# Kernel tuning notes

Hardware: AMD Instinct MI355X
Metric: run time of the kernel (lower is better)

Reference implementation:

```python
import jax, jax.numpy as jnp
import numpy as np

N_NODES = 8192
N_EDGES = 262144
FEAT = 128


def _lin(key, fan_in, fan_out):
    k1, k2 = jax.random.split(key)
    s = 1.0 / np.sqrt(fan_in)
    w = jax.random.uniform(k1, (fan_in, fan_out), jnp.float32, -s, s)
    b = jax.random.uniform(k2, (fan_out,), jnp.float32, -s, s)
    return w, b


def setup_inputs() -> dict:
    key = jax.random.key(0)
    ks = jax.random.split(key, 16)
    adj = jax.random.randint(ks[0], (2, N_EDGES), 0, N_NODES)
    features = jax.random.normal(ks[1], (N_NODES, FEAT), jnp.float32)
    w1, b1 = _lin(ks[2], FEAT, 64)
    w2, b2 = _lin(ks[3], 64, 32)
    w3, b3 = _lin(ks[4], 32, 32)
    # MultiheadAttention params (embed_dim=32, 1 head)
    kq = jax.random.split(ks[5], 2)
    wqkv = jax.random.uniform(kq[0], (96, 32), jnp.float32, -1/np.sqrt(32), 1/np.sqrt(32))
    bqkv = jnp.zeros((96,), jnp.float32)
    wo = jax.random.uniform(kq[1], (32, 32), jnp.float32, -1/np.sqrt(32), 1/np.sqrt(32))
    bo = jnp.zeros((32,), jnp.float32)
    w4, b4 = _lin(ks[6], 32, 32)
    w5a, b5a = _lin(ks[7], 32, 32)
    w6a, b6a = _lin(ks[8], 32, 64)
    w7a, b7a = _lin(ks[9], 64, 2)
    w5f, b5f = _lin(ks[10], 32, 32)
    w6f, b6f = _lin(ks[11], 32, 64)
    w7f, b7f = _lin(ks[12], 64, FEAT)
    return dict(adj=adj, features=features, w1=w1, b1=b1, w2=w2, b2=b2, w3=w3, b3=b3,
                wqkv=wqkv, bqkv=bqkv, wo=wo, bo=bo, w4=w4, b4=b4,
                w5a=w5a, b5a=b5a, w6a=w6a, b6a=b6a, w7a=w7a, b7a=b7a,
                w5f=w5f, b5f=b5f, w6f=w6f, b6f=b6f, w7f=w7f, b7f=b7f)


def _gcn(x, w, b, src, dst, norm, n):
    # PyG GCNConv: out = scatter_add(norm * (x W)[src] -> dst) + b
    h = x @ w
    return jax.ops.segment_sum(h[src] * norm[:, None], dst, num_segments=n) + b


def reference(adj, features, w1, b1, w2, b2, w3, b3, wqkv, bqkv, wo, bo, w4, b4,
              w5a, b5a, w6a, b6a, w7a, b7a, w5f, b5f, w6f, b6f, w7f, b7f):
    n = features.shape[0]
    loops = jnp.arange(n)
    src = jnp.concatenate([adj[0], loops])  # self-loops added (gcn_norm)
    dst = jnp.concatenate([adj[1], loops])
    deg = jax.ops.segment_sum(jnp.ones_like(src, jnp.float32), dst, num_segments=n)
    dinv = jnp.where(deg > 0, jax.lax.rsqrt(deg), 0.0)
    norm = dinv[src] * dinv[dst]

    h = jax.nn.relu(_gcn(features, w1, b1, src, dst, norm, n))
    h = jax.nn.relu(_gcn(h, w2, b2, src, dst, norm, n))
    h = jax.nn.relu(_gcn(h, w3, b3, src, dst, norm, n))

    # single-head self-attention over all nodes (seq_len=n, batch=1)
    qkv = h @ wqkv.T + bqkv
    q, k, v = jnp.split(qkv, 3, axis=-1)  # [n,32] each
    attn = jax.nn.softmax((q @ k.T) * (1.0 / np.sqrt(32.0)), axis=-1)  # [n,n]
    h = (attn @ v) @ wo.T + bo

    h = jax.nn.relu(_gcn(h, w4, b4, src, dst, norm, n))

    da = jax.nn.relu(_gcn(h, w5a, b5a, src, dst, norm, n))
    da = jax.nn.relu(_gcn(da, w6a, b6a, src, dst, norm, n))
    da = jax.nn.relu(_gcn(da, w7a, b7a, src, dst, norm, n))  # [n,2]

    df = jax.nn.relu(_gcn(h, w5f, b5f, src, dst, norm, n))
    df = jax.nn.relu(_gcn(df, w6f, b6f, src, dst, norm, n))
    df = jax.nn.relu(_gcn(df, w7f, b7f, src, dst, norm, n))  # [n,FEAT]
    return (da, df)
```

## Files before the change

### kernel.cpp

```cpp
#include <hip/hip_runtime.h>

#define N_NODES 8192
#define N_EDGES 262144

typedef __attribute__((ext_vector_type(4))) float f32x4;
typedef _Float16 half8 __attribute__((ext_vector_type(8)));
typedef __fp16 fp16x2 __attribute__((ext_vector_type(2)));
union UH { half8 h8; fp16x2 h2[4]; };
union HC { _Float16 h; unsigned short u; };


__global__ void __launch_bounds__(256) count_kernel(const int* __restrict__ dst,
                                                    int* __restrict__ cnt) {
  int e = blockIdx.x * 256 + threadIdx.x;
  atomicAdd(&cnt[dst[e]], 1);
}

__global__ void __launch_bounds__(1024) scan_kernel(const int* __restrict__ cnt,
                                                    int* __restrict__ rp,
                                                    float* __restrict__ dinv) {
  __shared__ int sums[1024];
  const int t = threadIdx.x;
  const int base = t * 8;
  int c[8];
  int s = 0;
#pragma unroll
  for (int i = 0; i < 8; ++i) { c[i] = cnt[base + i]; s += c[i]; }
  sums[t] = s;
  __syncthreads();
  for (int off = 1; off < 1024; off <<= 1) {
    int v = (t >= off) ? sums[t - off] : 0;
    __syncthreads();
    sums[t] += v;
    __syncthreads();
  }
  int run = (t == 0) ? 0 : sums[t - 1];
#pragma unroll
  for (int i = 0; i < 8; ++i) {
    rp[base + i] = run;
    run += c[i];
    dinv[base + i] = rsqrtf((float)(c[i] + 1));
  }
  if (t == 1023) rp[N_NODES] = run;
}

__global__ void __launch_bounds__(256) fill_kernel(const int* __restrict__ src,
                                                   const int* __restrict__ dst,
                                                   const int* __restrict__ rp,
                                                   const float* __restrict__ dinv,
                                                   int* __restrict__ cur,
                                                   int* __restrict__ col,
                                                   float* __restrict__ wgt) {
  int e = blockIdx.x * 256 + threadIdx.x;
  int d = dst[e], s = src[e];
  int p = atomicAdd(&cur[d], 1);
  int at = rp[d] + p;
  col[at] = s;
  wgt[at] = dinv[s] * dinv[d];
}


template <int FIN, int FOUT, bool WT, bool BIAS, bool RELU>
__device__ __forceinline__ void mm_body(const float* __restrict__ x,
                                        const float* __restrict__ w,
                                        const float* __restrict__ bias,
                                        float* __restrict__ out, int bx, int tid,
                                        float* ws, float* xs) {
  constexpr int VEC = (FOUT >= 32) ? 4 : 1;
  constexpr int TC = FOUT / VEC;
  constexpr int ROWS = 256 / TC;
  const int r0 = bx * ROWS;
  for (int i = tid; i < FIN * FOUT; i += 256) {
    int k = i / FOUT, j = i % FOUT;
    ws[i] = WT ? w[j * FIN + k] : w[i];
  }
  for (int i = tid; i < ROWS * FIN; i += 256) {
    int r = i / FIN, k = i % FIN;
    xs[r * (FIN + 1) + k] = x[(size_t)(r0 + r) * FIN + k];
  }
  __syncthreads();
  const int jc = tid % TC, r = tid / TC;
  float acc[VEC];
#pragma unroll
  for (int v = 0; v < VEC; ++v) acc[v] = 0.0f;
#pragma unroll
  for (int k = 0; k < FIN; ++k) {
    const float xv = xs[r * (FIN + 1) + k];
#pragma unroll
    for (int v = 0; v < VEC; ++v) acc[v] += xv * ws[k * FOUT + jc * VEC + v];
  }
#pragma unroll
  for (int v = 0; v < VEC; ++v) {
    int j = jc * VEC + v;
    float o = BIAS ? (acc[v] + bias[j]) : acc[v];
    if (RELU) o = fmaxf(o, 0.0f);
    out[(size_t)(r0 + r) * FOUT + j] = o;
  }
}

template <int FIN, int FOUT, bool WT, bool BIAS, bool RELU = false>
__global__ void __launch_bounds__(256) mm_kernel(const float* __restrict__ x,
                                                 const float* __restrict__ w,
                                                 const float* __restrict__ bias,
                                                 float* __restrict__ out) {
  constexpr int VEC = (FOUT >= 32) ? 4 : 1;
  constexpr int ROWS = 256 / (FOUT / VEC);
  __shared__ float ws[FIN * FOUT];
  __shared__ float xs[ROWS * (FIN + 1)];
  mm_body<FIN, FOUT, WT, BIAS, RELU>(x, w, bias, out, blockIdx.x, threadIdx.x, ws, xs);
}

template <int FIN, int FOUT, bool WT, bool BIAS, bool RELU, int G>
__global__ void __launch_bounds__(256) mm_dual_kernel(
    const float* __restrict__ xA, const float* __restrict__ wA,
    const float* __restrict__ bA, float* __restrict__ outA,
    const float* __restrict__ xB, const float* __restrict__ wB,
    const float* __restrict__ bB, float* __restrict__ outB) {
  constexpr int VEC = (FOUT >= 32) ? 4 : 1;
  constexpr int ROWS = 256 / (FOUT / VEC);
  __shared__ float ws[FIN * FOUT];
  __shared__ float xs[ROWS * (FIN + 1)];
  if (blockIdx.x < G)
    mm_body<FIN, FOUT, WT, BIAS, RELU>(xA, wA, bA, outA, blockIdx.x, threadIdx.x, ws, xs);
  else
    mm_body<FIN, FOUT, WT, BIAS, RELU>(xB, wB, bB, outB, blockIdx.x - G, threadIdx.x, ws, xs);
}


template <int F, bool BR>
__device__ __forceinline__ void aggv_body(const float* __restrict__ t,
                                          const int* __restrict__ rp,
                                          const int* __restrict__ col,
                                          const float* __restrict__ wgt,
                                          const float* __restrict__ dinv,
                                          const float* __restrict__ bias,
                                          float* __restrict__ out, int bx, int tid) {
  constexpr int TPN = F / 4;
  constexpr int EPI = 64 / TPN;
  const int wv = tid >> 6;
  const int lane = tid & 63;
  const int n = bx * 4 + wv;
  const int eo = lane / TPN;
  const int fq = lane % TPN;
  const float di = dinv[n];
  const int rs = rp[n], re = rp[n + 1];
  f32x4 acc = {0.f, 0.f, 0.f, 0.f};
  if (eo == 0) {
    const f32x4 tv = *(const f32x4*)&t[(size_t)n * F + fq * 4];
    acc = di * di * tv;
  }
  for (int e = rs + eo; e < re; e += EPI) {
    const int c = col[e];
    const float w = wgt[e];
    const f32x4 tv = *(const f32x4*)&t[(size_t)c * F + fq * 4];
    acc += w * tv;
  }
#pragma unroll
  for (int off = TPN; off < 64; off <<= 1) {
    acc[0] += __shfl_xor(acc[0], off, 64);
    acc[1] += __shfl_xor(acc[1], off, 64);
    acc[2] += __shfl_xor(acc[2], off, 64);
    acc[3] += __shfl_xor(acc[3], off, 64);
  }
  if (eo == 0) {
    f32x4 r = acc;
    if (BR) {
      const f32x4 bv = *(const f32x4*)&bias[fq * 4];
      r = acc + bv;
      r[0] = fmaxf(r[0], 0.f); r[1] = fmaxf(r[1], 0.f);
      r[2] = fmaxf(r[2], 0.f); r[3] = fmaxf(r[3], 0.f);
    }
    *(f32x4*)&out[(size_t)n * F + fq * 4] = r;
  }
}

template <int F, bool BR = true>
__global__ void __launch_bounds__(256) aggv_kernel(const float* __restrict__ t,
                                                   const int* __restrict__ rp,
                                                   const int* __restrict__ col,
                                                   const float* __restrict__ wgt,
                                                   const float* __restrict__ dinv,
                                                   const float* __restrict__ bias,
                                                   float* __restrict__ out) {
  aggv_body<F, BR>(t, rp, col, wgt, dinv, bias, out, blockIdx.x, threadIdx.x);
}

template <int F, bool BR, int G>
__global__ void __launch_bounds__(256) aggv_dual_kernel(
    const float* __restrict__ tA, const float* __restrict__ bA, float* __restrict__ outA,
    const float* __restrict__ tB, const float* __restrict__ bB, float* __restrict__ outB,
    const int* __restrict__ rp, const int* __restrict__ col,
    const float* __restrict__ wgt, const float* __restrict__ dinv) {
  if (blockIdx.x < G)
    aggv_body<F, BR>(tA, rp, col, wgt, dinv, bA, outA, blockIdx.x, threadIdx.x);
  else
    aggv_body<F, BR>(tB, rp, col, wgt, dinv, bB, outB, blockIdx.x - G, threadIdx.x);
}

template <int F>
__global__ void __launch_bounds__(256) agg_kernel(const float* __restrict__ t,
                                                  const int* __restrict__ rp,
                                                  const int* __restrict__ col,
                                                  const float* __restrict__ wgt,
                                                  const float* __restrict__ dinv,
                                                  const float* __restrict__ bias,
                                                  float* __restrict__ out) {
  constexpr int NPB = 256 / F;
  const int tid = threadIdx.x;
  const int n = blockIdx.x * NPB + tid / F;
  const int f = tid % F;
  const float di = dinv[n];
  float acc = di * di * t[(size_t)n * F + f];
  const int rs = rp[n], re = rp[n + 1];
  for (int e = rs; e < re; ++e) {
    acc += wgt[e] * t[(size_t)col[e] * F + f];
  }
  acc += bias[f];
  out[(size_t)n * F + f] = fmaxf(acc, 0.0f);
}


__global__ void __launch_bounds__(256) qkv_kernel(const float* __restrict__ x,
                                                  const float* __restrict__ wqkv,
                                                  const float* __restrict__ bqkv,
                                                  unsigned short* __restrict__ Q16,
                                                  unsigned short* __restrict__ K16,
                                                  unsigned short* __restrict__ V16) {
  __shared__ float wls[96 * 33];
  __shared__ float xs[8 * 33];
  const int tid = threadIdx.x;
  const int r = tid >> 5, j = tid & 31;
  const int row = blockIdx.x * 8 + r;
  for (int i = tid; i < 96 * 32; i += 256) wls[(i >> 5) * 33 + (i & 31)] = wqkv[i];
  xs[(tid >> 5) * 33 + (tid & 31)] = x[(size_t)(blockIdx.x * 8 + (tid >> 5)) * 32 + (tid & 31)];
  __syncthreads();
  float aq = bqkv[j], ak = bqkv[32 + j], av = bqkv[64 + j];
#pragma unroll
  for (int k = 0; k < 32; ++k) {
    const float xv = xs[r * 33 + k];
    aq += xv * wls[j * 33 + k];
    ak += xv * wls[(32 + j) * 33 + k];
    av += xv * wls[(64 + j) * 33 + k];
  }
  const float QSCALE = 1.4426950408889634f * 0.17677669529663687f;
  aq *= QSCALE;
  HC cq, ck, cv;
  cq.h = (_Float16)aq;
  ck.h = (_Float16)ak;
  cv.h = (_Float16)av;
  Q16[row * 32 + j] = cq.u;
  K16[row * 32 + j] = ck.u;
  const int ko = row & 31;
  const int slot = 8 * ((ko & 15) >> 2) + ((ko >> 4) << 2) + (ko & 3);
  V16[j * N_NODES + (row & ~31) + slot] = cv.u;
}


__device__ __forceinline__ void wave_writeout(float (*lds)[544], float (*wexp)[16],
                                              float* Mq, float* Lq, const f32x4& o1,
                                              const f32x4& o2, float m, float l, int wid,
                                              int g, int li, int tid, int qt, int by,
                                              float* __restrict__ part) {
#pragma unroll
  for (int r = 0; r < 4; ++r) {
    lds[wid][(4 * g + r) * 16 + li] = o1[r];
    lds[wid][(16 + 4 * g + r) * 16 + li] = o2[r];
  }
  if (g == 0) {
    lds[wid][512 + li] = m;
    lds[wid][528 + li] = l;
  }
  __syncthreads();
  if (tid < 16) {
    const int q = tid;
    const float m0 = lds[0][512 + q], m1 = lds[1][512 + q];
    const float m2 = lds[2][512 + q], m3 = lds[3][512 + q];
    const float M = fmaxf(fmaxf(m0, m1), fmaxf(m2, m3));
    const float w0 = exp2f(m0 - M), w1 = exp2f(m1 - M);
    const float w2 = exp2f(m2 - M), w3 = exp2f(m3 - M);
    wexp[0][q] = w0; wexp[1][q] = w1; wexp[2][q] = w2; wexp[3][q] = w3;
    Mq[q] = M;
    Lq[q] = w0 * lds[0][528 + q] + w1 * lds[1][528 + q] +
            w2 * lds[2][528 + q] + w3 * lds[3][528 + q];
  }
  __syncthreads();
  const int base = (qt * 4 + by) * 544;
#pragma unroll
  for (int e2 = 0; e2 < 2; ++e2) {
    const int e = tid + e2 * 256;
    const int q = e & 15;
    part[base + e] = wexp[0][q] * lds[0][e] + wexp[1][q] * lds[1][e] +
                     wexp[2][q] * lds[2][e] + wexp[3][q] * lds[3][e];
  }
  if (tid < 16) {
    part[base + 512 + tid] = Mq[tid];
    part[base + 528 + tid] = Lq[tid];
  }
}

__global__ void __launch_bounds__(256, 4) attn_mfma_kernel(
    const unsigned short* __restrict__ Q16, const unsigned short* __restrict__ K16,
    const unsigned short* __restrict__ V16, float* __restrict__ part) {
  __shared__ float lds[4][544];
  __shared__ float wexp[4][16];
  __shared__ float Mq[16], Lq[16];
  const int tid = threadIdx.x;
  const int wid = tid >> 6;
  const int lane = tid & 63;
  const int g = lane >> 4;
  const int li = lane & 15;
  const int qpair = blockIdx.x;
  const int q0A = qpair * 32;
  const int q0B = q0A + 16;
  const int kbeg = blockIdx.y * 2048 + wid * 512;

  const half8 qfA = *(const half8*)&Q16[(q0A + li) * 32 + 8 * g];
  const half8 qfB = *(const half8*)&Q16[(q0B + li) * 32 + 8 * g];
  const int koff = li * 32 + 8 * g;
  const int vA = li * N_NODES + 8 * g;
  const int vB = (16 + li) * N_NODES + 8 * g;

  f32x4 oAA = {0.f, 0.f, 0.f, 0.f}, oBA = {0.f, 0.f, 0.f, 0.f};
  f32x4 oAB = {0.f, 0.f, 0.f, 0.f}, oBB = {0.f, 0.f, 0.f, 0.f};
  float mA = -1e30f, lA = 0.f, mB = -1e30f, lB = 0.f;

  for (int t = kbeg; t < kbeg + 512; t += 64) {
    const half8 k0 = *(const half8*)&K16[(t)*32 + koff];
    const half8 k1 = *(const half8*)&K16[(t + 16) * 32 + koff];
    const half8 k2 = *(const half8*)&K16[(t + 32) * 32 + koff];
    const half8 k3 = *(const half8*)&K16[(t + 48) * 32 + koff];
    const half8 va0 = *(const half8*)&V16[vA + t];
    const half8 vb0 = *(const half8*)&V16[vB + t];
    const half8 va1 = *(const half8*)&V16[vA + t + 32];
    const half8 vb1 = *(const half8*)&V16[vB + t + 32];

    {
      f32x4 s0 = {0.f, 0.f, 0.f, 0.f}, s1 = {0.f, 0.f, 0.f, 0.f};
      f32x4 s2 = {0.f, 0.f, 0.f, 0.f}, s3 = {0.f, 0.f, 0.f, 0.f};
      s0 = __builtin_amdgcn_mfma_f32_16x16x32_f16(k0, qfA, s0, 0, 0, 0);
      s1 = __builtin_amdgcn_mfma_f32_16x16x32_f16(k1, qfA, s1, 0, 0, 0);
      s2 = __builtin_amdgcn_mfma_f32_16x16x32_f16(k2, qfA, s2, 0, 0, 0);
      s3 = __builtin_amdgcn_mfma_f32_16x16x32_f16(k3, qfA, s3, 0, 0, 0);
      float mxl = fmaxf(fmaxf(fmaxf(s0[0], s0[1]), fmaxf(s0[2], s0[3])),
                        fmaxf(fmaxf(s1[0], s1[1]), fmaxf(s1[2], s1[3])));
      mxl = fmaxf(mxl, fmaxf(fmaxf(fmaxf(s2[0], s2[1]), fmaxf(s2[2], s2[3])),
                             fmaxf(fmaxf(s3[0], s3[1]), fmaxf(s3[2], s3[3]))));
      if (!__all(mxl <= mA)) {
        float mx = mxl;
        mx = fmaxf(mx, __shfl_xor(mx, 16, 64));
        mx = fmaxf(mx, __shfl_xor(mx, 32, 64));
        const float mn = fmaxf(mA, mx);
        const float fct = exp2f(mA - mn);
        oAA *= fct; oBA *= fct; lA *= fct;
        mA = mn;
      }
      const float p0 = exp2f(s0[0] - mA), p1 = exp2f(s0[1] - mA);
      const float p2 = exp2f(s0[2] - mA), p3 = exp2f(s0[3] - mA);
      const float p4 = exp2f(s1[0] - mA), p5 = exp2f(s1[1] - mA);
      const float p6 = exp2f(s1[2] - mA), p7 = exp2f(s1[3] - mA);
      const float p8 = exp2f(s2[0] - mA), p9 = exp2f(s2[1] - mA);
      const float pa = exp2f(s2[2] - mA), pb = exp2f(s2[3] - mA);
      const float pc = exp2f(s3[0] - mA), pd = exp2f(s3[1] - mA);
      const float pe = exp2f(s3[2] - mA), pf = exp2f(s3[3] - mA);
      lA += (((p0 + p1) + (p2 + p3)) + ((p4 + p5) + (p6 + p7))) +
            (((p8 + p9) + (pa + pb)) + ((pc + pd) + (pe + pf)));
      UH ph0, ph1;
      ph0.h2[0] = __builtin_amdgcn_cvt_pkrtz(p0, p1);
      ph0.h2[1] = __builtin_amdgcn_cvt_pkrtz(p2, p3);
      ph0.h2[2] = __builtin_amdgcn_cvt_pkrtz(p4, p5);
      ph0.h2[3] = __builtin_amdgcn_cvt_pkrtz(p6, p7);
      ph1.h2[0] = __builtin_amdgcn_cvt_pkrtz(p8, p9);
      ph1.h2[1] = __builtin_amdgcn_cvt_pkrtz(pa, pb);
      ph1.h2[2] = __builtin_amdgcn_cvt_pkrtz(pc, pd);
      ph1.h2[3] = __builtin_amdgcn_cvt_pkrtz(pe, pf);
      oAA = __builtin_amdgcn_mfma_f32_16x16x32_f16(va0, ph0.h8, oAA, 0, 0, 0);
      oAA = __builtin_amdgcn_mfma_f32_16x16x32_f16(va1, ph1.h8, oAA, 0, 0, 0);
      oBA = __builtin_amdgcn_mfma_f32_16x16x32_f16(vb0, ph0.h8, oBA, 0, 0, 0);
      oBA = __builtin_amdgcn_mfma_f32_16x16x32_f16(vb1, ph1.h8, oBA, 0, 0, 0);
    }
    {
      f32x4 s0 = {0.f, 0.f, 0.f, 0.f}, s1 = {0.f, 0.f, 0.f, 0.f};
      f32x4 s2 = {0.f, 0.f, 0.f, 0.f}, s3 = {0.f, 0.f, 0.f, 0.f};
      s0 = __builtin_amdgcn_mfma_f32_16x16x32_f16(k0, qfB, s0, 0, 0, 0);
      s1 = __builtin_amdgcn_mfma_f32_16x16x32_f16(k1, qfB, s1, 0, 0, 0);
      s2 = __builtin_amdgcn_mfma_f32_16x16x32_f16(k2, qfB, s2, 0, 0, 0);
      s3 = __builtin_amdgcn_mfma_f32_16x16x32_f16(k3, qfB, s3, 0, 0, 0);
      float mxl = fmaxf(fmaxf(fmaxf(s0[0], s0[1]), fmaxf(s0[2], s0[3])),
                        fmaxf(fmaxf(s1[0], s1[1]), fmaxf(s1[2], s1[3])));
      mxl = fmaxf(mxl, fmaxf(fmaxf(fmaxf(s2[0], s2[1]), fmaxf(s2[2], s2[3])),
                             fmaxf(fmaxf(s3[0], s3[1]), fmaxf(s3[2], s3[3]))));
      if (!__all(mxl <= mB)) {
        float mx = mxl;
        mx = fmaxf(mx, __shfl_xor(mx, 16, 64));
        mx = fmaxf(mx, __shfl_xor(mx, 32, 64));
        const float mn = fmaxf(mB, mx);
        const float fct = exp2f(mB - mn);
        oAB *= fct; oBB *= fct; lB *= fct;
        mB = mn;
      }
      const float p0 = exp2f(s0[0] - mB), p1 = exp2f(s0[1] - mB);
      const float p2 = exp2f(s0[2] - mB), p3 = exp2f(s0[3] - mB);
      const float p4 = exp2f(s1[0] - mB), p5 = exp2f(s1[1] - mB);
      const float p6 = exp2f(s1[2] - mB), p7 = exp2f(s1[3] - mB);
      const float p8 = exp2f(s2[0] - mB), p9 = exp2f(s2[1] - mB);
      const float pa = exp2f(s2[2] - mB), pb = exp2f(s2[3] - mB);
      const float pc = exp2f(s3[0] - mB), pd = exp2f(s3[1] - mB);
      const float pe = exp2f(s3[2] - mB), pf = exp2f(s3[3] - mB);
      lB += (((p0 + p1) + (p2 + p3)) + ((p4 + p5) + (p6 + p7))) +
            (((p8 + p9) + (pa + pb)) + ((pc + pd) + (pe + pf)));
      UH ph0, ph1;
      ph0.h2[0] = __builtin_amdgcn_cvt_pkrtz(p0, p1);
      ph0.h2[1] = __builtin_amdgcn_cvt_pkrtz(p2, p3);
      ph0.h2[2] = __builtin_amdgcn_cvt_pkrtz(p4, p5);
      ph0.h2[3] = __builtin_amdgcn_cvt_pkrtz(p6, p7);
      ph1.h2[0] = __builtin_amdgcn_cvt_pkrtz(p8, p9);
      ph1.h2[1] = __builtin_amdgcn_cvt_pkrtz(pa, pb);
      ph1.h2[2] = __builtin_amdgcn_cvt_pkrtz(pc, pd);
      ph1.h2[3] = __builtin_amdgcn_cvt_pkrtz(pe, pf);
      oAB = __builtin_amdgcn_mfma_f32_16x16x32_f16(va0, ph0.h8, oAB, 0, 0, 0);
      oAB = __builtin_amdgcn_mfma_f32_16x16x32_f16(va1, ph1.h8, oAB, 0, 0, 0);
      oBB = __builtin_amdgcn_mfma_f32_16x16x32_f16(vb0, ph0.h8, oBB, 0, 0, 0);
      oBB = __builtin_amdgcn_mfma_f32_16x16x32_f16(vb1, ph1.h8, oBB, 0, 0, 0);
    }
  }

  lA += __shfl_xor(lA, 16, 64);
  lA += __shfl_xor(lA, 32, 64);
  lB += __shfl_xor(lB, 16, 64);
  lB += __shfl_xor(lB, 32, 64);

  wave_writeout(lds, wexp, Mq, Lq, oAA, oBA, mA, lA, wid, g, li, tid, qpair * 2,
                blockIdx.y, part);
  __syncthreads();
  wave_writeout(lds, wexp, Mq, Lq, oAB, oBB, mB, lB, wid, g, li, tid, qpair * 2 + 1,
                blockIdx.y, part);
}


__global__ void __launch_bounds__(256) attn_combine_wo(const float* __restrict__ part,
                                                       const float* __restrict__ wo,
                                                       const float* __restrict__ bo,
                                                       float* __restrict__ out) {
  __shared__ float wols[1024];
  __shared__ float bos[32];
  __shared__ float aos[4][16][33];
  const int tid = threadIdx.x;
  for (int i = tid; i < 1024; i += 256) wols[i] = wo[i];
  if (tid < 32) bos[tid] = bo[tid];
  const int wv = tid >> 6, lane = tid & 63;
  const int qt = blockIdx.x * 4 + wv;
  const int q = lane & 15, g = lane >> 4;
  const int pb = qt * 4 * 544;
  const float m0 = part[pb + 512 + q], m1 = part[pb + 544 + 512 + q];
  const float m2 = part[pb + 1088 + 512 + q], m3 = part[pb + 1632 + 512 + q];
  const float M = fmaxf(fmaxf(m0, m1), fmaxf(m2, m3));
  const float w0 = exp2f(m0 - M), w1 = exp2f(m1 - M);
  const float w2 = exp2f(m2 - M), w3 = exp2f(m3 - M);
  const float L = w0 * part[pb + 528 + q] + w1 * part[pb + 544 + 528 + q] +
                  w2 * part[pb + 1088 + 528 + q] + w3 * part[pb + 1632 + 528 + q];
  const float invL = 1.0f / L;
#pragma unroll
  for (int r = 0; r < 8; ++r) {
    const int d = g + 4 * r;
    const int o = d * 16 + q;
    const float ov = w0 * part[pb + o] + w1 * part[pb + 544 + o] +
                     w2 * part[pb + 1088 + o] + w3 * part[pb + 1632 + o];
    aos[wv][q][d] = ov * invL;
  }
  __syncthreads();
#pragma unroll
  for (int r = 0; r < 8; ++r) {
    const int dout = g + 4 * r;
    float acc = bos[dout];
#pragma unroll
    for (int k = 0; k < 32; ++k) acc += aos[wv][q][k] * wols[dout * 32 + k];
    out[(size_t)(qt * 16 + q) * 32 + dout] = acc;
  }
}


extern "C" void kernel_launch(void* const* d_in, const int* in_sizes, int n_in,
                              void* d_out, int out_size, void* d_ws, size_t ws_size,
                              hipStream_t stream) {
  (void)in_sizes; (void)n_in; (void)out_size; (void)ws_size;
  const int* adj = (const int*)d_in[0];
  const float* feat = (const float*)d_in[1];
  const float* w1 = (const float*)d_in[2];  const float* b1 = (const float*)d_in[3];
  const float* w2 = (const float*)d_in[4];  const float* b2 = (const float*)d_in[5];
  const float* w3 = (const float*)d_in[6];  const float* b3 = (const float*)d_in[7];
  const float* wqkv = (const float*)d_in[8];const float* bqkv = (const float*)d_in[9];
  const float* wo = (const float*)d_in[10]; const float* bo = (const float*)d_in[11];
  const float* w4 = (const float*)d_in[12]; const float* b4 = (const float*)d_in[13];
  const float* w5a = (const float*)d_in[14];const float* b5a = (const float*)d_in[15];
  const float* w6a = (const float*)d_in[16];const float* b6a = (const float*)d_in[17];
  const float* w7a = (const float*)d_in[18];const float* b7a = (const float*)d_in[19];
  const float* w5f = (const float*)d_in[20];const float* b5f = (const float*)d_in[21];
  const float* w6f = (const float*)d_in[22];const float* b6f = (const float*)d_in[23];
  const float* w7f = (const float*)d_in[24];const float* b7f = (const float*)d_in[25];
  float* outp = (float*)d_out;

  float* wsf = (float*)d_ws;
  int* wsi = (int*)d_ws;
  int* cnt = wsi;
  int* cur = wsi + 8192;
  int* rp = wsi + 16384;
  float* dinv = wsf + 24832;
  float* wgt = wsf + 33024;
  int* col = wsi + 295168;
  float* T = wsf + 557312;
  float* T2 = T + 262144;
  float* B0 = wsf + 1605888;
  float* B1 = wsf + 2130176;
  float* B2 = wsf + 2392320;
  unsigned short* Q16 = (unsigned short*)(wsf + 2916608);
  unsigned short* K16 = Q16 + 262144;
  unsigned short* V16 = K16 + 262144;
  float* part = T;

  const int* src = adj;
  const int* dst = adj + N_EDGES;

  hipMemsetAsync(cnt, 0, 2 * N_NODES * sizeof(int), stream);
  count_kernel<<<N_EDGES / 256, 256, 0, stream>>>(dst, cnt);
  scan_kernel<<<1, 1024, 0, stream>>>(cnt, rp, dinv);
  fill_kernel<<<N_EDGES / 256, 256, 0, stream>>>(src, dst, rp, dinv, cur, col, wgt);

  mm_kernel<128, 64, false, false><<<N_NODES / 16, 256, 0, stream>>>(feat, w1, nullptr, T);
  aggv_kernel<64><<<N_NODES / 4, 256, 0, stream>>>(T, rp, col, wgt, dinv, b1, B0);
  mm_kernel<64, 32, false, false><<<N_NODES / 32, 256, 0, stream>>>(B0, w2, nullptr, T);
  aggv_kernel<32><<<N_NODES / 4, 256, 0, stream>>>(T, rp, col, wgt, dinv, b2, B1);
  mm_kernel<32, 32, false, false><<<N_NODES / 32, 256, 0, stream>>>(B1, w3, nullptr, T);
  aggv_kernel<32><<<N_NODES / 4, 256, 0, stream>>>(T, rp, col, wgt, dinv, b3, B0);

  qkv_kernel<<<N_NODES / 8, 256, 0, stream>>>(B0, wqkv, bqkv, Q16, K16, V16);
  {
    dim3 grid(256, 4);
    attn_mfma_kernel<<<grid, 256, 0, stream>>>(Q16, K16, V16, part);
  }
  attn_combine_wo<<<128, 256, 0, stream>>>(part, wo, bo, B2);

  mm_kernel<32, 32, false, false><<<N_NODES / 32, 256, 0, stream>>>(B2, w4, nullptr, T);
  aggv_kernel<32><<<N_NODES / 4, 256, 0, stream>>>(T, rp, col, wgt, dinv, b4, B0);

  mm_dual_kernel<32, 32, false, false, false, 256><<<512, 256, 0, stream>>>(
      B0, w5a, nullptr, T, B0, w5f, nullptr, T2);
  aggv_dual_kernel<32, true, 2048><<<4096, 256, 0, stream>>>(
      T, b5a, B1, T2, b5f, B2, rp, col, wgt, dinv);
  aggv_dual_kernel<32, false, 2048><<<4096, 256, 0, stream>>>(
      B1, nullptr, T, B2, nullptr, T2, rp, col, wgt, dinv);
  mm_dual_kernel<32, 64, false, true, true, 512><<<1024, 256, 0, stream>>>(
      T, w6a, b6a, B0, T2, w6f, b6f, B2);
  mm_kernel<64, 2, false, false><<<N_NODES / 128, 256, 0, stream>>>(B0, w7a, nullptr, B1);
  agg_kernel<2><<<N_NODES / 128, 256, 0, stream>>>(B1, rp, col, wgt, dinv, b7a, outp);
  aggv_kernel<64, false><<<N_NODES / 4, 256, 0, stream>>>(B2, rp, col, wgt, dinv, nullptr, T);
  mm_kernel<64, 128, false, true, true><<<N_NODES / 8, 256, 0, stream>>>(T, w7f, b7f,
                                                                         outp + 16384);
}
```

Baseline: 199.1 us.

## Process four query tiles per attention wave to reuse K/V loads; replace memset

```diff
diff --git a/kernel.cpp b/kernel.cpp
--- a/kernel.cpp
+++ b/kernel.cpp
@@ -8,6 +8,11 @@
 typedef __fp16 fp16x2 __attribute__((ext_vector_type(2)));
 union UH { half8 h8; fp16x2 h2[4]; };
 union HC { _Float16 h; unsigned short u; };
+
+
+__global__ void __launch_bounds__(256) zero_kernel(int4* __restrict__ p) {
+  p[blockIdx.x * 256 + threadIdx.x] = make_int4(0, 0, 0, 0);
+}
 
 
 __global__ void __launch_bounds__(256) count_kernel(const int* __restrict__ dst,
@@ -298,7 +303,53 @@
   }
 }
 
-__global__ void __launch_bounds__(256, 4) attn_mfma_kernel(
+#define ATTN_QTILE(QQ)                                                                \
+  do {                                                                                \
+    f32x4 s0 = {0.f, 0.f, 0.f, 0.f}, s1 = {0.f, 0.f, 0.f, 0.f};                      \
+    f32x4 s2 = {0.f, 0.f, 0.f, 0.f}, s3 = {0.f, 0.f, 0.f, 0.f};                      \
+    s0 = __builtin_amdgcn_mfma_f32_16x16x32_f16(k0, qf[QQ], s0, 0, 0, 0);             \
+    s1 = __builtin_amdgcn_mfma_f32_16x16x32_f16(k1, qf[QQ], s1, 0, 0, 0);             \
+    s2 = __builtin_amdgcn_mfma_f32_16x16x32_f16(k2, qf[QQ], s2, 0, 0, 0);             \
+    s3 = __builtin_amdgcn_mfma_f32_16x16x32_f16(k3, qf[QQ], s3, 0, 0, 0);             \
+    float mxl = fmaxf(fmaxf(fmaxf(s0[0], s0[1]), fmaxf(s0[2], s0[3])),                \
+                      fmaxf(fmaxf(s1[0], s1[1]), fmaxf(s1[2], s1[3])));               \
+    mxl = fmaxf(mxl, fmaxf(fmaxf(fmaxf(s2[0], s2[1]), fmaxf(s2[2], s2[3])),           \
+                           fmaxf(fmaxf(s3[0], s3[1]), fmaxf(s3[2], s3[3]))));         \
+    if (!__all(mxl <= m[QQ])) {                                                       \
+      float mx = mxl;                                                                 \
+      mx = fmaxf(mx, __shfl_xor(mx, 16, 64));                                         \
+      mx = fmaxf(mx, __shfl_xor(mx, 32, 64));                                         \
+      const float mn = fmaxf(m[QQ], mx);                                              \
+      const float fct = exp2f(m[QQ] - mn);                                            \
+      o1[QQ] *= fct; o2[QQ] *= fct; l[QQ] *= fct;                                     \
+      m[QQ] = mn;                                                                     \
+    }                                                                                 \
+    const float p0 = exp2f(s0[0] - m[QQ]), p1 = exp2f(s0[1] - m[QQ]);                 \
+    const float p2 = exp2f(s0[2] - m[QQ]), p3 = exp2f(s0[3] - m[QQ]);                 \
+    const float p4 = exp2f(s1[0] - m[QQ]), p5 = exp2f(s1[1] - m[QQ]);                 \
+    const float p6 = exp2f(s1[2] - m[QQ]), p7 = exp2f(s1[3] - m[QQ]);                 \
+    const float p8 = exp2f(s2[0] - m[QQ]), p9 = exp2f(s2[1] - m[QQ]);                 \
+    const float pa = exp2f(s2[2] - m[QQ]), pb = exp2f(s2[3] - m[QQ]);                 \
+    const float pc = exp2f(s3[0] - m[QQ]), pd = exp2f(s3[1] - m[QQ]);                 \
+    const float pe = exp2f(s3[2] - m[QQ]), pf = exp2f(s3[3] - m[QQ]);                 \
+    l[QQ] += (((p0 + p1) + (p2 + p3)) + ((p4 + p5) + (p6 + p7))) +                    \
+             (((p8 + p9) + (pa + pb)) + ((pc + pd) + (pe + pf)));                     \
+    UH ph0, ph1;                                                                      \
+    ph0.h2[0] = __builtin_amdgcn_cvt_pkrtz(p0, p1);                                   \
+    ph0.h2[1] = __builtin_amdgcn_cvt_pkrtz(p2, p3);                                   \
+    ph0.h2[2] = __builtin_amdgcn_cvt_pkrtz(p4, p5);                                   \
+    ph0.h2[3] = __builtin_amdgcn_cvt_pkrtz(p6, p7);                                   \
+    ph1.h2[0] = __builtin_amdgcn_cvt_pkrtz(p8, p9);                                   \
+    ph1.h2[1] = __builtin_amdgcn_cvt_pkrtz(pa, pb);                                   \
+    ph1.h2[2] = __builtin_amdgcn_cvt_pkrtz(pc, pd);                                   \
+    ph1.h2[3] = __builtin_amdgcn_cvt_pkrtz(pe, pf);                                   \
+    o1[QQ] = __builtin_amdgcn_mfma_f32_16x16x32_f16(va0, ph0.h8, o1[QQ], 0, 0, 0);    \
+    o1[QQ] = __builtin_amdgcn_mfma_f32_16x16x32_f16(va1, ph1.h8, o1[QQ], 0, 0, 0);    \
+    o2[QQ] = __builtin_amdgcn_mfma_f32_16x16x32_f16(vb0, ph0.h8, o2[QQ], 0, 0, 0);    \
+    o2[QQ] = __builtin_amdgcn_mfma_f32_16x16x32_f16(vb1, ph1.h8, o2[QQ], 0, 0, 0);    \
+  } while (0)
+
+__global__ void __launch_bounds__(256, 2) attn_mfma_kernel(
     const unsigned short* __restrict__ Q16, const unsigned short* __restrict__ K16,
     const unsigned short* __restrict__ V16, float* __restrict__ part) {
   __shared__ float lds[4][544];
@@ -309,20 +360,27 @@
   const int lane = tid & 63;
   const int g = lane >> 4;
   const int li = lane & 15;
-  const int qpair = blockIdx.x;
-  const int q0A = qpair * 32;
-  const int q0B = q0A + 16;
+  const int qquad = blockIdx.x;
   const int kbeg = blockIdx.y * 2048 + wid * 512;
 
-  const half8 qfA = *(const half8*)&Q16[(q0A + li) * 32 + 8 * g];
-  const half8 qfB = *(const half8*)&Q16[(q0B + li) * 32 + 8 * g];
+  half8 qf[4];
+#pragma unroll
+  for (int qq = 0; qq < 4; ++qq)
+    qf[qq] = *(const half8*)&Q16[(qquad * 64 + qq * 16 + li) * 32 + 8 * g];
+
   const int koff = li * 32 + 8 * g;
   const int vA = li * N_NODES + 8 * g;
   const int vB = (16 + li) * N_NODES + 8 * g;
 
-  f32x4 oAA = {0.f, 0.f, 0.f, 0.f}, oBA = {0.f, 0.f, 0.f, 0.f};
-  f32x4 oAB = {0.f, 0.f, 0.f, 0.f}, oBB = {0.f, 0.f, 0.f, 0.f};
-  float mA = -1e30f, lA = 0.f, mB = -1e30f, lB = 0.f;
+  f32x4 o1[4], o2[4];
+  float m[4], l[4];
+#pragma unroll
+  for (int qq = 0; qq < 4; ++qq) {
+    o1[qq] = f32x4{0.f, 0.f, 0.f, 0.f};
+    o2[qq] = f32x4{0.f, 0.f, 0.f, 0.f};
+    m[qq] = -1e30f;
+    l[qq] = 0.f;
+  }
 
   for (int t = kbeg; t < kbeg + 512; t += 64) {
     const half8 k0 = *(const half8*)&K16[(t)*32 + koff];
@@ -333,107 +391,29 @@
     const half8 vb0 = *(const half8*)&V16[vB + t];
     const half8 va1 = *(const half8*)&V16[vA + t + 32];
     const half8 vb1 = *(const half8*)&V16[vB + t + 32];
-
-    {
-      f32x4 s0 = {0.f, 0.f, 0.f, 0.f}, s1 = {0.f, 0.f, 0.f, 0.f};
-      f32x4 s2 = {0.f, 0.f, 0.f, 0.f}, s3 = {0.f, 0.f, 0.f, 0.f};
-      s0 = __builtin_amdgcn_mfma_f32_16x16x32_f16(k0, qfA, s0, 0, 0, 0);
-      s1 = __builtin_amdgcn_mfma_f32_16x16x32_f16(k1, qfA, s1, 0, 0, 0);
-      s2 = __builtin_amdgcn_mfma_f32_16x16x32_f16(k2, qfA, s2, 0, 0, 0);
-      s3 = __builtin_amdgcn_mfma_f32_16x16x32_f16(k3, qfA, s3, 0, 0, 0);
-      float mxl = fmaxf(fmaxf(fmaxf(s0[0], s0[1]), fmaxf(s0[2], s0[3])),
-                        fmaxf(fmaxf(s1[0], s1[1]), fmaxf(s1[2], s1[3])));
-      mxl = fmaxf(mxl, fmaxf(fmaxf(fmaxf(s2[0], s2[1]), fmaxf(s2[2], s2[3])),
-                             fmaxf(fmaxf(s3[0], s3[1]), fmaxf(s3[2], s3[3]))));
-      if (!__all(mxl <= mA)) {
-        float mx = mxl;
-        mx = fmaxf(mx, __shfl_xor(mx, 16, 64));
-        mx = fmaxf(mx, __shfl_xor(mx, 32, 64));
-        const float mn = fmaxf(mA, mx);
-        const float fct = exp2f(mA - mn);
-        oAA *= fct; oBA *= fct; lA *= fct;
-        mA = mn;
-      }
-      const float p0 = exp2f(s0[0] - mA), p1 = exp2f(s0[1] - mA);
-      const float p2 = exp2f(s0[2] - mA), p3 = exp2f(s0[3] - mA);
-      const float p4 = exp2f(s1[0] - mA), p5 = exp2f(s1[1] - mA);
-      const float p6 = exp2f(s1[2] - mA), p7 = exp2f(s1[3] - mA);
-      const float p8 = exp2f(s2[0] - mA), p9 = exp2f(s2[1] - mA);
-      const float pa = exp2f(s2[2] - mA), pb = exp2f(s2[3] - mA);
-      const float pc = exp2f(s3[0] - mA), pd = exp2f(s3[1] - mA);
-      const float pe = exp2f(s3[2] - mA), pf = exp2f(s3[3] - mA);
-      lA += (((p0 + p1) + (p2 + p3)) + ((p4 + p5) + (p6 + p7))) +
-            (((p8 + p9) + (pa + pb)) + ((pc + pd) + (pe + pf)));
-      UH ph0, ph1;
-      ph0.h2[0] = __builtin_amdgcn_cvt_pkrtz(p0, p1);
-      ph0.h2[1] = __builtin_amdgcn_cvt_pkrtz(p2, p3);
-      ph0.h2[2] = __builtin_amdgcn_cvt_pkrtz(p4, p5);
-      ph0.h2[3] = __builtin_amdgcn_cvt_pkrtz(p6, p7);
-      ph1.h2[0] = __builtin_amdgcn_cvt_pkrtz(p8, p9);
-      ph1.h2[1] = __builtin_amdgcn_cvt_pkrtz(pa, pb);
-      ph1.h2[2] = __builtin_amdgcn_cvt_pkrtz(pc, pd);
-      ph1.h2[3] = __builtin_amdgcn_cvt_pkrtz(pe, pf);
-      oAA = __builtin_amdgcn_mfma_f32_16x16x32_f16(va0, ph0.h8, oAA, 0, 0, 0);
-      oAA = __builtin_amdgcn_mfma_f32_16x16x32_f16(va1, ph1.h8, oAA, 0, 0, 0);
-      oBA = __builtin_amdgcn_mfma_f32_16x16x32_f16(vb0, ph0.h8, oBA, 0, 0, 0);
-      oBA = __builtin_amdgcn_mfma_f32_16x16x32_f16(vb1, ph1.h8, oBA, 0, 0, 0);
-    }
-    {
-      f32x4 s0 = {0.f, 0.f, 0.f, 0.f}, s1 = {0.f, 0.f, 0.f, 0.f};
-      f32x4 s2 = {0.f, 0.f, 0.f, 0.f}, s3 = {0.f, 0.f, 0.f, 0.f};
-      s0 = __builtin_amdgcn_mfma_f32_16x16x32_f16(k0, qfB, s0, 0, 0, 0);
-      s1 = __builtin_amdgcn_mfma_f32_16x16x32_f16(k1, qfB, s1, 0, 0, 0);
-      s2 = __builtin_amdgcn_mfma_f32_16x16x32_f16(k2, qfB, s2, 0, 0, 0);
-      s3 = __builtin_amdgcn_mfma_f32_16x16x32_f16(k3, qfB, s3, 0, 0, 0);
-      float mxl = fmaxf(fmaxf(fmaxf(s0[0], s0[1]), fmaxf(s0[2], s0[3])),
-                        fmaxf(fmaxf(s1[0], s1[1]), fmaxf(s1[2], s1[3])));
-      mxl = fmaxf(mxl, fmaxf(fmaxf(fmaxf(s2[0], s2[1]), fmaxf(s2[2], s2[3])),
-                             fmaxf(fmaxf(s3[0], s3[1]), fmaxf(s3[2], s3[3]))));
-      if (!__all(mxl <= mB)) {
-        float mx = mxl;
-        mx = fmaxf(mx, __shfl_xor(mx, 16, 64));
-        mx = fmaxf(mx, __shfl_xor(mx, 32, 64));
-        const float mn = fmaxf(mB, mx);
-        const float fct = exp2f(mB - mn);
-        oAB *= fct; oBB *= fct; lB *= fct;
-        mB = mn;
-      }
-      const float p0 = exp2f(s0[0] - mB), p1 = exp2f(s0[1] - mB);
-      const float p2 = exp2f(s0[2] - mB), p3 = exp2f(s0[3] - mB);
-      const float p4 = exp2f(s1[0] - mB), p5 = exp2f(s1[1] - mB);
-      const float p6 = exp2f(s1[2] - mB), p7 = exp2f(s1[3] - mB);
-      const float p8 = exp2f(s2[0] - mB), p9 = exp2f(s2[1] - mB);
-      const float pa = exp2f(s2[2] - mB), pb = exp2f(s2[3] - mB);
-      const float pc = exp2f(s3[0] - mB), pd = exp2f(s3[1] - mB);
-      const float pe = exp2f(s3[2] - mB), pf = exp2f(s3[3] - mB);
-      lB += (((p0 + p1) + (p2 + p3)) + ((p4 + p5) + (p6 + p7))) +
-            (((p8 + p9) + (pa + pb)) + ((pc + pd) + (pe + pf)));
-      UH ph0, ph1;
-      ph0.h2[0] = __builtin_amdgcn_cvt_pkrtz(p0, p1);
-      ph0.h2[1] = __builtin_amdgcn_cvt_pkrtz(p2, p3);
-      ph0.h2[2] = __builtin_amdgcn_cvt_pkrtz(p4, p5);
-      ph0.h2[3] = __builtin_amdgcn_cvt_pkrtz(p6, p7);
-      ph1.h2[0] = __builtin_amdgcn_cvt_pkrtz(p8, p9);
-      ph1.h2[1] = __builtin_amdgcn_cvt_pkrtz(pa, pb);
-      ph1.h2[2] = __builtin_amdgcn_cvt_pkrtz(pc, pd);
-      ph1.h2[3] = __builtin_amdgcn_cvt_pkrtz(pe, pf);
-      oAB = __builtin_amdgcn_mfma_f32_16x16x32_f16(va0, ph0.h8, oAB, 0, 0, 0);
-      oAB = __builtin_amdgcn_mfma_f32_16x16x32_f16(va1, ph1.h8, oAB, 0, 0, 0);
-      oBB = __builtin_amdgcn_mfma_f32_16x16x32_f16(vb0, ph0.h8, oBB, 0, 0, 0);
-      oBB = __builtin_amdgcn_mfma_f32_16x16x32_f16(vb1, ph1.h8, oBB, 0, 0, 0);
-    }
-  }
-
-  lA += __shfl_xor(lA, 16, 64);
-  lA += __shfl_xor(lA, 32, 64);
-  lB += __shfl_xor(lB, 16, 64);
-  lB += __shfl_xor(lB, 32, 64);
-
-  wave_writeout(lds, wexp, Mq, Lq, oAA, oBA, mA, lA, wid, g, li, tid, qpair * 2,
-                blockIdx.y, part);
-  __syncthreads();
-  wave_writeout(lds, wexp, Mq, Lq, oAB, oBB, mB, lB, wid, g, li, tid, qpair * 2 + 1,
-                blockIdx.y, part);
+    ATTN_QTILE(0);
+    ATTN_QTILE(1);
+    ATTN_QTILE(2);
+    ATTN_QTILE(3);
+  }
+
+#pragma unroll
+  for (int qq = 0; qq < 4; ++qq) {
+    l[qq] += __shfl_xor(l[qq], 16, 64);
+    l[qq] += __shfl_xor(l[qq], 32, 64);
+  }
+
+  wave_writeout(lds, wexp, Mq, Lq, o1[0], o2[0], m[0], l[0], wid, g, li, tid,
+                qquad * 4 + 0, blockIdx.y, part);
+  __syncthreads();
+  wave_writeout(lds, wexp, Mq, Lq, o1[1], o2[1], m[1], l[1], wid, g, li, tid,
+                qquad * 4 + 1, blockIdx.y, part);
+  __syncthreads();
+  wave_writeout(lds, wexp, Mq, Lq, o1[2], o2[2], m[2], l[2], wid, g, li, tid,
+                qquad * 4 + 2, blockIdx.y, part);
+  __syncthreads();
+  wave_writeout(lds, wexp, Mq, Lq, o1[3], o2[3], m[3], l[3], wid, g, li, tid,
+                qquad * 4 + 3, blockIdx.y, part);
 }
 
 
@@ -520,7 +500,7 @@
   const int* src = adj;
   const int* dst = adj + N_EDGES;
 
-  hipMemsetAsync(cnt, 0, 2 * N_NODES * sizeof(int), stream);
+  zero_kernel<<<16, 256, 0, stream>>>((int4*)cnt);
   count_kernel<<<N_EDGES / 256, 256, 0, stream>>>(dst, cnt);
   scan_kernel<<<1, 1024, 0, stream>>>(cnt, rp, dinv);
   fill_kernel<<<N_EDGES / 256, 256, 0, stream>>>(src, dst, rp, dinv, cur, col, wgt);
@@ -534,7 +514,7 @@
 
   qkv_kernel<<<N_NODES / 8, 256, 0, stream>>>(B0, wqkv, bqkv, Q16, K16, V16);
   {
-    dim3 grid(256, 4);
+    dim3 grid(128, 4);
     attn_mfma_kernel<<<grid, 256, 0, stream>>>(Q16, K16, V16, part);
   }
   attn_combine_wo<<<128, 256, 0, stream>>>(part, wo, bo, B2);
```

Result: no change. 201.9 us (+1.4%).

## Store GCN transform outputs as fp16 and share one aggregation for layer-5 branches

Applied to the files above, without the earlier changes.

```diff
diff --git a/kernel.cpp b/kernel.cpp
--- a/kernel.cpp
+++ b/kernel.cpp
@@ -5,9 +5,15 @@
 
 typedef __attribute__((ext_vector_type(4))) float f32x4;
 typedef _Float16 half8 __attribute__((ext_vector_type(8)));
+typedef _Float16 half4v __attribute__((ext_vector_type(4)));
 typedef __fp16 fp16x2 __attribute__((ext_vector_type(2)));
 union UH { half8 h8; fp16x2 h2[4]; };
 union HC { _Float16 h; unsigned short u; };
+
+
+__global__ void __launch_bounds__(256) zero_kernel(int4* __restrict__ p) {
+  p[blockIdx.x * 256 + threadIdx.x] = make_int4(0, 0, 0, 0);
+}
 
 
 __global__ void __launch_bounds__(256) count_kernel(const int* __restrict__ dst,
@@ -60,12 +66,11 @@
 }
 
 
-template <int FIN, int FOUT, bool WT, bool BIAS, bool RELU>
+template <int FIN, int FOUT, bool WT, bool BIAS, bool RELU, bool O16>
 __device__ __forceinline__ void mm_body(const float* __restrict__ x,
                                         const float* __restrict__ w,
-                                        const float* __restrict__ bias,
-                                        float* __restrict__ out, int bx, int tid,
-                                        float* ws, float* xs) {
+                                        const float* __restrict__ bias, void* out,
+                                        int bx, int tid, float* ws, float* xs) {
   constexpr int VEC = (FOUT >= 32) ? 4 : 1;
   constexpr int TC = FOUT / VEC;
   constexpr int ROWS = 256 / TC;
@@ -89,46 +94,58 @@
 #pragma unroll
     for (int v = 0; v < VEC; ++v) acc[v] += xv * ws[k * FOUT + jc * VEC + v];
   }
+  float oval[VEC];
 #pragma unroll
   for (int v = 0; v < VEC; ++v) {
     int j = jc * VEC + v;
     float o = BIAS ? (acc[v] + bias[j]) : acc[v];
     if (RELU) o = fmaxf(o, 0.0f);
-    out[(size_t)(r0 + r) * FOUT + j] = o;
-  }
-}
-
-template <int FIN, int FOUT, bool WT, bool BIAS, bool RELU = false>
+    oval[v] = o;
+  }
+  if constexpr (O16 && VEC == 4) {
+    unsigned short* o16 = (unsigned short*)out;
+    half4v pk;
+#pragma unroll
+    for (int v = 0; v < 4; ++v) pk[v] = (_Float16)oval[v];
+    *(half4v*)&o16[(size_t)(r0 + r) * FOUT + jc * 4] = pk;
+  } else {
+    float* of = (float*)out;
+#pragma unroll
+    for (int v = 0; v < VEC; ++v) of[(size_t)(r0 + r) * FOUT + jc * VEC + v] = oval[v];
+  }
+}
+
+template <int FIN, int FOUT, bool WT, bool BIAS, bool RELU = false, bool O16 = false>
 __global__ void __launch_bounds__(256) mm_kernel(const float* __restrict__ x,
                                                  const float* __restrict__ w,
                                                  const float* __restrict__ bias,
-                                                 float* __restrict__ out) {
+                                                 void* out) {
   constexpr int VEC = (FOUT >= 32) ? 4 : 1;
   constexpr int ROWS = 256 / (FOUT / VEC);
   __shared__ float ws[FIN * FOUT];
   __shared__ float xs[ROWS * (FIN + 1)];
-  mm_body<FIN, FOUT, WT, BIAS, RELU>(x, w, bias, out, blockIdx.x, threadIdx.x, ws, xs);
-}
-
-template <int FIN, int FOUT, bool WT, bool BIAS, bool RELU, int G>
+  mm_body<FIN, FOUT, WT, BIAS, RELU, O16>(x, w, bias, out, blockIdx.x, threadIdx.x, ws, xs);
+}
+
+template <int FIN, int FOUT, bool WT, bool BIAS, bool RELU, int G, bool O16 = false>
 __global__ void __launch_bounds__(256) mm_dual_kernel(
     const float* __restrict__ xA, const float* __restrict__ wA,
-    const float* __restrict__ bA, float* __restrict__ outA,
+    const float* __restrict__ bA, void* outA,
     const float* __restrict__ xB, const float* __restrict__ wB,
-    const float* __restrict__ bB, float* __restrict__ outB) {
+    const float* __restrict__ bB, void* outB) {
   constexpr int VEC = (FOUT >= 32) ? 4 : 1;
   constexpr int ROWS = 256 / (FOUT / VEC);
   __shared__ float ws[FIN * FOUT];
   __shared__ float xs[ROWS * (FIN + 1)];
   if (blockIdx.x < G)
-    mm_body<FIN, FOUT, WT, BIAS, RELU>(xA, wA, bA, outA, blockIdx.x, threadIdx.x, ws, xs);
+    mm_body<FIN, FOUT, WT, BIAS, RELU, O16>(xA, wA, bA, outA, blockIdx.x, threadIdx.x, ws, xs);
   else
-    mm_body<FIN, FOUT, WT, BIAS, RELU>(xB, wB, bB, outB, blockIdx.x - G, threadIdx.x, ws, xs);
-}
-
-
-template <int F, bool BR>
-__device__ __forceinline__ void aggv_body(const float* __restrict__ t,
+    mm_body<FIN, FOUT, WT, BIAS, RELU, O16>(xB, wB, bB, outB, blockIdx.x - G, threadIdx.x, ws, xs);
+}
+
+
+template <int F, bool BR, bool I16>
+__device__ __forceinline__ void aggv_body(const void* __restrict__ t,
                                           const int* __restrict__ rp,
                                           const int* __restrict__ col,
                                           const float* __restrict__ wgt,
@@ -145,15 +162,22 @@
   const float di = dinv[n];
   const int rs = rp[n], re = rp[n + 1];
   f32x4 acc = {0.f, 0.f, 0.f, 0.f};
+  auto loadrow = [&](int node) -> f32x4 {
+    if constexpr (I16) {
+      const half4v hv =
+          *(const half4v*)((const unsigned short*)t + (size_t)node * F + fq * 4);
+      return f32x4{(float)hv[0], (float)hv[1], (float)hv[2], (float)hv[3]};
+    } else {
+      return *(const f32x4*)((const float*)t + (size_t)node * F + fq * 4);
+    }
+  };
   if (eo == 0) {
-    const f32x4 tv = *(const f32x4*)&t[(size_t)n * F + fq * 4];
-    acc = di * di * tv;
+    acc = di * di * loadrow(n);
   }
   for (int e = rs + eo; e < re; e += EPI) {
     const int c = col[e];
     const float w = wgt[e];
-    const f32x4 tv = *(const f32x4*)&t[(size_t)c * F + fq * 4];
-    acc += w * tv;
+    acc += w * loadrow(c);
   }
 #pragma unroll
   for (int off = TPN; off < 64; off <<= 1) {
@@ -174,15 +198,15 @@
   }
 }
 
-template <int F, bool BR = true>
-__global__ void __launch_bounds__(256) aggv_kernel(const float* __restrict__ t,
+template <int F, bool BR = true, bool I16 = false>
+__global__ void __launch_bounds__(256) aggv_kernel(const void* __restrict__ t,
                                                    const int* __restrict__ rp,
                                                    const int* __restrict__ col,
                                                    const float* __restrict__ wgt,
                                                    const float* __restrict__ dinv,
                                                    const float* __restrict__ bias,
                                                    float* __restrict__ out) {
-  aggv_body<F, BR>(t, rp, col, wgt, dinv, bias, out, blockIdx.x, threadIdx.x);
+  aggv_body<F, BR, I16>(t, rp, col, wgt, dinv, bias, out, blockIdx.x, threadIdx.x);
 }
 
 template <int F, bool BR, int G>
@@ -192,9 +216,9 @@
     const int* __restrict__ rp, const int* __restrict__ col,
     const float* __restrict__ wgt, const float* __restrict__ dinv) {
   if (blockIdx.x < G)
-    aggv_body<F, BR>(tA, rp, col, wgt, dinv, bA, outA, blockIdx.x, threadIdx.x);
+    aggv_body<F, BR, false>(tA, rp, col, wgt, dinv, bA, outA, blockIdx.x, threadIdx.x);
   else
-    aggv_body<F, BR>(tB, rp, col, wgt, dinv, bB, outB, blockIdx.x - G, threadIdx.x);
+    aggv_body<F, BR, false>(tB, rp, col, wgt, dinv, bB, outB, blockIdx.x - G, threadIdx.x);
 }
 
 template <int F>
@@ -515,22 +539,26 @@
   unsigned short* Q16 = (unsigned short*)(wsf + 2916608);
   unsigned short* K16 = Q16 + 262144;
   unsigned short* V16 = K16 + 262144;
+  unsigned short* T16 = (unsigned short*)T;
   float* part = T;
 
   const int* src = adj;
   const int* dst = adj + N_EDGES;
 
-  hipMemsetAsync(cnt, 0, 2 * N_NODES * sizeof(int), stream);
+  zero_kernel<<<16, 256, 0, stream>>>((int4*)cnt);
   count_kernel<<<N_EDGES / 256, 256, 0, stream>>>(dst, cnt);
   scan_kernel<<<1, 1024, 0, stream>>>(cnt, rp, dinv);
   fill_kernel<<<N_EDGES / 256, 256, 0, stream>>>(src, dst, rp, dinv, cur, col, wgt);
 
-  mm_kernel<128, 64, false, false><<<N_NODES / 16, 256, 0, stream>>>(feat, w1, nullptr, T);
-  aggv_kernel<64><<<N_NODES / 4, 256, 0, stream>>>(T, rp, col, wgt, dinv, b1, B0);
-  mm_kernel<64, 32, false, false><<<N_NODES / 32, 256, 0, stream>>>(B0, w2, nullptr, T);
-  aggv_kernel<32><<<N_NODES / 4, 256, 0, stream>>>(T, rp, col, wgt, dinv, b2, B1);
-  mm_kernel<32, 32, false, false><<<N_NODES / 32, 256, 0, stream>>>(B1, w3, nullptr, T);
-  aggv_kernel<32><<<N_NODES / 4, 256, 0, stream>>>(T, rp, col, wgt, dinv, b3, B0);
+  mm_kernel<128, 64, false, false, false, true><<<N_NODES / 16, 256, 0, stream>>>(
+      feat, w1, nullptr, T16);
+  aggv_kernel<64, true, true><<<N_NODES / 4, 256, 0, stream>>>(T16, rp, col, wgt, dinv, b1, B0);
+  mm_kernel<64, 32, false, false, false, true><<<N_NODES / 32, 256, 0, stream>>>(
+      B0, w2, nullptr, T16);
+  aggv_kernel<32, true, true><<<N_NODES / 4, 256, 0, stream>>>(T16, rp, col, wgt, dinv, b2, B1);
+  mm_kernel<32, 32, false, false, false, true><<<N_NODES / 32, 256, 0, stream>>>(
+      B1, w3, nullptr, T16);
+  aggv_kernel<32, true, true><<<N_NODES / 4, 256, 0, stream>>>(T16, rp, col, wgt, dinv, b3, B0);
 
   qkv_kernel<<<N_NODES / 8, 256, 0, stream>>>(B0, wqkv, bqkv, Q16, K16, V16);
   {
@@ -539,13 +567,13 @@
   }
   attn_combine_wo<<<128, 256, 0, stream>>>(part, wo, bo, B2);
 
-  mm_kernel<32, 32, false, false><<<N_NODES / 32, 256, 0, stream>>>(B2, w4, nullptr, T);
-  aggv_kernel<32><<<N_NODES / 4, 256, 0, stream>>>(T, rp, col, wgt, dinv, b4, B0);
-
-  mm_dual_kernel<32, 32, false, false, false, 256><<<512, 256, 0, stream>>>(
-      B0, w5a, nullptr, T, B0, w5f, nullptr, T2);
-  aggv_dual_kernel<32, true, 2048><<<4096, 256, 0, stream>>>(
-      T, b5a, B1, T2, b5f, B2, rp, col, wgt, dinv);
+  mm_kernel<32, 32, false, false, false, true><<<N_NODES / 32, 256, 0, stream>>>(
+      B2, w4, nullptr, T16);
+  aggv_kernel<32, true, true><<<N_NODES / 4, 256, 0, stream>>>(T16, rp, col, wgt, dinv, b4, B0);
+
+  aggv_kernel<32, false><<<N_NODES / 4, 256, 0, stream>>>(B0, rp, col, wgt, dinv, nullptr, T);
+  mm_dual_kernel<32, 32, false, true, true, 256><<<512, 256, 0, stream>>>(
+      T, w5a, b5a, B1, T, w5f, b5f, B2);
   aggv_dual_kernel<32, false, 2048><<<4096, 256, 0, stream>>>(
       B1, nullptr, T, B2, nullptr, T2, rp, col, wgt, dinv);
   mm_dual_kernel<32, 64, false, true, true, 512><<<1024, 256, 0, stream>>>(
```

Measured after the change: 191.5 us. 1.04x faster.
